# Performance work log

Hardware: AMD Instinct MI355X
Metric: run time of the kernel (lower is better)

The kernel has to match this reference:

```python
import jax, jax.numpy as jnp
import numpy as np

N = 10000       # nodes
E = 320000      # edges (before self-loops)
IN = 16         # in_channels


def _p(key, shape, scale=0.1):
    return jax.random.normal(key, shape, jnp.float32) * scale


def setup_inputs() -> dict:
    key = jax.random.key(0)
    ks = jax.random.split(key, 26)
    d = {}
    d["x"] = jax.random.normal(ks[0], (N, IN), jnp.float32)
    d["edge_index"] = jax.random.randint(ks[1], (2, E), 0, N, jnp.int32)
    d["JetRawPt"] = jax.random.normal(ks[2], (N, 1), jnp.float32)
    # conv1: GATConv(16 -> 32, heads=8)
    d["W1"] = _p(ks[3], (IN, 8 * 32)); d["a1s"] = _p(ks[4], (8, 32)); d["a1d"] = _p(ks[5], (8, 32)); d["b1"] = jnp.zeros((256,), jnp.float32)
    # conv2: GATConv(256 -> 32, heads=8)
    d["W2"] = _p(ks[6], (256, 8 * 32)); d["a2s"] = _p(ks[7], (8, 32)); d["a2d"] = _p(ks[8], (8, 32)); d["b2"] = jnp.zeros((256,), jnp.float32)
    # conv3: GATConv(256 -> 64, heads=12)
    d["W3"] = _p(ks[9], (256, 12 * 64)); d["a3s"] = _p(ks[10], (12, 64)); d["a3d"] = _p(ks[11], (12, 64)); d["b3"] = jnp.zeros((768,), jnp.float32)
    # linear_final: 256+256+768=1280 -> 1
    d["Wf"] = _p(ks[12], (1280, 1)); d["bf"] = jnp.zeros((1,), jnp.float32)
    # MLP: (16+1)->128->64->1
    d["M1w"] = _p(ks[13], (IN + 1, 128)); d["M1b"] = jnp.zeros((128,), jnp.float32)
    d["M2w"] = _p(ks[14], (128, 64)); d["M2b"] = jnp.zeros((64,), jnp.float32)
    d["M3w"] = _p(ks[15], (64, 1)); d["M3b"] = jnp.zeros((1,), jnp.float32)
    return d


def gat_layer(x, src, dst, W, a_s, a_d, b, H, C):
    # PyG GATConv (eval mode, self-loops already appended to src/dst)
    h = (x @ W).reshape(-1, H, C)                      # [N, H, C]
    al = jnp.sum(h * a_s, axis=-1)                     # [N, H] src-side score
    ar = jnp.sum(h * a_d, axis=-1)                     # [N, H] dst-side score
    e = jax.nn.leaky_relu(al[src] + ar[dst], 0.2)      # [Etot, H]
    m = jax.ops.segment_max(e, dst, num_segments=N)    # segment softmax over incoming edges
    ex = jnp.exp(e - m[dst])
    s = jax.ops.segment_sum(ex, dst, num_segments=N)
    alpha = ex / s[dst]                                # [Etot, H]
    out = jax.ops.segment_sum(h[src] * alpha[:, :, None], dst, num_segments=N)  # [N, H, C]
    return out.reshape(-1, H * C) + b


def reference(x, edge_index, JetRawPt, W1, a1s, a1d, b1, W2, a2s, a2d, b2,
              W3, a3s, a3d, b3, Wf, bf, M1w, M1b, M2w, M2b, M3w, M3b):
    loops = jnp.arange(N, dtype=edge_index.dtype)
    src = jnp.concatenate([edge_index[0], loops])
    dst = jnp.concatenate([edge_index[1], loops])
    x1 = jax.nn.relu(gat_layer(x, src, dst, W1, a1s, a1d, b1, 8, 32))
    x2 = jax.nn.relu(gat_layer(x1, src, dst, W2, a2s, a2d, b2, 8, 32))
    x3 = jax.nn.relu(gat_layer(x2, src, dst, W3, a3s, a3d, b3, 12, 64))
    xc = jnp.concatenate([x1, x2, x3], axis=1)         # [N, 1280]
    out1 = jax.nn.sigmoid(xc @ Wf + bf)                # [N, 1]
    xm = jnp.concatenate([x, out1], axis=1)            # [N, 17]
    h = jax.nn.relu(xm @ M1w + M1b)
    h = jax.nn.relu(h @ M2w + M2b)
    out2 = jax.nn.sigmoid(h @ M3w + M3b)               # [N, 1]
    return (out1, out2)
```

## Files before the change

### kernel.cpp

```cpp
#include <hip/hip_runtime.h>
#include <math.h>


typedef unsigned short bf16_t;
typedef __attribute__((ext_vector_type(8))) short bf16x8;
typedef __attribute__((ext_vector_type(4))) float f32x4;
typedef __attribute__((ext_vector_type(2))) float f32x2;

__device__ inline float bf2f(bf16_t u) {
    union { unsigned int i; float f; } v; v.i = ((unsigned int)u) << 16; return v.f;
}
__device__ inline float u2f(unsigned int x) {
    union { unsigned int i; float f; } v; v.i = x; return v.f;
}
__device__ inline bf16_t f2bf(float f) {
    union { float f; unsigned int i; } v; v.f = f;
    unsigned int r = v.i + 0x7FFF + ((v.i >> 16) & 1);
    return (bf16_t)(r >> 16);
}


__global__ void count_edges(const int* __restrict__ ei, int E, int Nn,
                            int* __restrict__ counts) {
    int e = blockIdx.x * blockDim.x + threadIdx.x;
    if (e >= E + Nn) return;
    int dst = (e < E) ? ei[E + e] : (e - E);
    atomicAdd(&counts[dst], 1);
}

__global__ __launch_bounds__(1024) void scan_rowptr(const int* __restrict__ counts,
                                                    int* __restrict__ rowptr, int n) {
    const int IPT = (n + 1023) / 1024;
    int t = threadIdx.x;
    int base = t * IPT;
    int loc[16];
    int run = 0;
#pragma unroll
    for (int i = 0; i < 16; i++) {
        if (i >= IPT) break;
        int idx = base + i;
        int v = (idx < n) ? counts[idx] : 0;
        loc[i] = run;
        run += v;
    }
    int lane = t & 63, wid = t >> 6;
    int v = run;
    for (int off = 1; off < 64; off <<= 1) {
        int u = __shfl_up(v, off, 64);
        if (lane >= off) v += u;
    }
    __shared__ int wsum[16];
    __shared__ int woff[16];
    if (lane == 63) wsum[wid] = v;
    __syncthreads();
    if (t == 0) { int s = 0; for (int i = 0; i < 16; i++) { woff[i] = s; s += wsum[i]; } }
    __syncthreads();
    int excl = v - run + woff[wid];
#pragma unroll
    for (int i = 0; i < 16; i++) {
        if (i >= IPT) break;
        int idx = base + i;
        if (idx < n) rowptr[idx] = excl + loc[i];
    }
    if (t == 1023) rowptr[n] = excl + run;
}

__global__ void fill_edges(const int* __restrict__ ei, int E, int Nn,
                           const int* __restrict__ rowptr, int* __restrict__ cursor,
                           int* __restrict__ edge_src) {
    int e = blockIdx.x * blockDim.x + threadIdx.x;
    if (e >= E + Nn) return;
    int src, dst;
    if (e < E) { src = ei[e]; dst = ei[E + e]; }
    else       { src = e - E; dst = src; }
    int pos = atomicAdd(&cursor[dst], 1);
    edge_src[rowptr[dst] + pos] = src;
}

__global__ __launch_bounds__(256) void transpose_cast2(const float* __restrict__ W2,
                                                       bf16_t* __restrict__ Wt2,
                                                       const float* __restrict__ W3,
                                                       bf16_t* __restrict__ Wt3) {
    __shared__ float tile[16][17];
    const float* W; bf16_t* Wt; int Nc, n0;
    if (blockIdx.y < 16) { W = W2; Wt = Wt2; Nc = 256; n0 = blockIdx.y * 16; }
    else                 { W = W3; Wt = Wt3; Nc = 768; n0 = (blockIdx.y - 16) * 16; }
    int k0 = blockIdx.x * 16;
    int tx = threadIdx.x & 15, ty = threadIdx.x >> 4;
    tile[ty][tx] = W[(size_t)(k0 + ty) * Nc + n0 + tx];
    __syncthreads();
    Wt[(size_t)(n0 + ty) * 256 + k0 + tx] = f2bf(tile[tx][ty]);
}

__global__ __launch_bounds__(256) void gemm_f32_sc(const float* __restrict__ A,
                                                   const float* __restrict__ B,
                                                   bf16_t* __restrict__ Cm,
                                                   const float* __restrict__ a_s,
                                                   const float* __restrict__ a_d,
                                                   float* __restrict__ al,
                                                   float* __restrict__ ar,
                                                   int M, int K, int Nc, int H) {
    __shared__ float As[16][64];
    __shared__ float Bs[16][64];
    int t  = threadIdx.x;
    int tx = t & 15, ty = t >> 4;
    int row0 = blockIdx.y * 64, col0 = blockIdx.x * 64;
    int a_r = t >> 2, a_c = (t & 3) * 4;
    int b_r = t >> 4, b_c = (t & 15) * 4;

    float acc[4][4];
#pragma unroll
    for (int i = 0; i < 4; i++)
#pragma unroll
        for (int j = 0; j < 4; j++) acc[i][j] = 0.f;

    for (int kt = 0; kt < K; kt += 16) {
        float4 av = make_float4(0.f, 0.f, 0.f, 0.f);
        int gr = row0 + a_r;
        if (gr < M) av = *(const float4*)(A + (size_t)gr * K + kt + a_c);
        As[a_c + 0][a_r] = av.x;
        As[a_c + 1][a_r] = av.y;
        As[a_c + 2][a_r] = av.z;
        As[a_c + 3][a_r] = av.w;
        float4 bv = *(const float4*)(B + (size_t)(kt + b_r) * Nc + col0 + b_c);
        *(float4*)&Bs[b_r][b_c] = bv;
        __syncthreads();
#pragma unroll
        for (int k = 0; k < 16; k++) {
            float4 a4 = *(const float4*)&As[k][ty * 4];
            float4 b4 = *(const float4*)&Bs[k][tx * 4];
            float aa[4] = {a4.x, a4.y, a4.z, a4.w};
            float bb[4] = {b4.x, b4.y, b4.z, b4.w};
#pragma unroll
            for (int i = 0; i < 4; i++)
#pragma unroll
                for (int j = 0; j < 4; j++) acc[i][j] += aa[i] * bb[j];
        }
        __syncthreads();
    }
    float4 asv = *(const float4*)(a_s + col0 + tx * 4);
    float4 adv = *(const float4*)(a_d + col0 + tx * 4);
#pragma unroll
    for (int i = 0; i < 4; i++) {
        int gr = row0 + ty * 4 + i;
        float sa = acc[i][0] * asv.x + acc[i][1] * asv.y + acc[i][2] * asv.z + acc[i][3] * asv.w;
        float sd = acc[i][0] * adv.x + acc[i][1] * adv.y + acc[i][2] * adv.z + acc[i][3] * adv.w;
#pragma unroll
        for (int off = 4; off > 0; off >>= 1) {
            sa += __shfl_xor(sa, off, 64);
            sd += __shfl_xor(sd, off, 64);
        }
        if ((tx == 0 || tx == 8) && gr < M) {
            int h = (col0 >> 5) + (tx >> 3);
            al[gr * H + h] = sa;
            ar[gr * H + h] = sd;
        }
        if (gr < M) {
            ushort4 v;
            v.x = f2bf(acc[i][0]); v.y = f2bf(acc[i][1]);
            v.z = f2bf(acc[i][2]); v.w = f2bf(acc[i][3]);
            *(ushort4*)(Cm + (size_t)gr * Nc + col0 + tx * 4) = v;
        }
    }
}

template <int C_>
__global__ __launch_bounds__(256) void gemm_mfma_sc(const bf16_t* __restrict__ A,
                                                    const bf16_t* __restrict__ Bt,
                                                    bf16_t* __restrict__ Cm,
                                                    const float* __restrict__ a_s,
                                                    const float* __restrict__ a_d,
                                                    float* __restrict__ al,
                                                    float* __restrict__ ar,
                                                    int M, int K, int Nc, int H) {
    int wave = threadIdx.x >> 6, lane = threadIdx.x & 63;
    int quad = lane >> 4, l16 = lane & 15;
    int m0 = blockIdx.y * 128 + wave * 32;
    int n0 = blockIdx.x * 64;

    f32x4 acc[2][4];
    f32x4 z = {0.f, 0.f, 0.f, 0.f};
#pragma unroll
    for (int i = 0; i < 2; i++)
#pragma unroll
        for (int j = 0; j < 4; j++) acc[i][j] = z;

    int r0 = m0 + l16;       if (r0 >= M) r0 = M - 1;
    int r1 = m0 + 16 + l16;  if (r1 >= M) r1 = M - 1;
    const bf16_t* Ap0 = A + (size_t)r0 * K + quad * 8;
    const bf16_t* Ap1 = A + (size_t)r1 * K + quad * 8;
    const bf16_t* Bp0 = Bt + (size_t)(n0 + 0  + l16) * K + quad * 8;
    const bf16_t* Bp1 = Bt + (size_t)(n0 + 16 + l16) * K + quad * 8;
    const bf16_t* Bp2 = Bt + (size_t)(n0 + 32 + l16) * K + quad * 8;
    const bf16_t* Bp3 = Bt + (size_t)(n0 + 48 + l16) * K + quad * 8;

    for (int kt = 0; kt < K; kt += 32) {
        bf16x8 a0 = *(const bf16x8*)(Ap0 + kt);
        bf16x8 a1 = *(const bf16x8*)(Ap1 + kt);
        bf16x8 b0 = *(const bf16x8*)(Bp0 + kt);
        bf16x8 b1 = *(const bf16x8*)(Bp1 + kt);
        bf16x8 b2 = *(const bf16x8*)(Bp2 + kt);
        bf16x8 b3 = *(const bf16x8*)(Bp3 + kt);
        acc[0][0] = __builtin_amdgcn_mfma_f32_16x16x32_bf16(a0, b0, acc[0][0], 0, 0, 0);
        acc[1][0] = __builtin_amdgcn_mfma_f32_16x16x32_bf16(a1, b0, acc[1][0], 0, 0, 0);
        acc[0][1] = __builtin_amdgcn_mfma_f32_16x16x32_bf16(a0, b1, acc[0][1], 0, 0, 0);
        acc[1][1] = __builtin_amdgcn_mfma_f32_16x16x32_bf16(a1, b1, acc[1][1], 0, 0, 0);
        acc[0][2] = __builtin_amdgcn_mfma_f32_16x16x32_bf16(a0, b2, acc[0][2], 0, 0, 0);
        acc[1][2] = __builtin_amdgcn_mfma_f32_16x16x32_bf16(a1, b2, acc[1][2], 0, 0, 0);
        acc[0][3] = __builtin_amdgcn_mfma_f32_16x16x32_bf16(a0, b3, acc[0][3], 0, 0, 0);
        acc[1][3] = __builtin_amdgcn_mfma_f32_16x16x32_bf16(a1, b3, acc[1][3], 0, 0, 0);
    }

    float asv[4], adv[4];
#pragma unroll
    for (int j = 0; j < 4; j++) {
        asv[j] = a_s[n0 + j * 16 + l16];
        adv[j] = a_d[n0 + j * 16 + l16];
    }
#pragma unroll
    for (int i = 0; i < 2; i++)
#pragma unroll
        for (int r = 0; r < 4; r++) {
            int gr = m0 + i * 16 + quad * 4 + r;
            if (C_ == 64) {
                float sa = acc[i][0][r] * asv[0] + acc[i][1][r] * asv[1]
                         + acc[i][2][r] * asv[2] + acc[i][3][r] * asv[3];
                float sd = acc[i][0][r] * adv[0] + acc[i][1][r] * adv[1]
                         + acc[i][2][r] * adv[2] + acc[i][3][r] * adv[3];
#pragma unroll
                for (int off = 8; off > 0; off >>= 1) {
                    sa += __shfl_xor(sa, off, 64);
                    sd += __shfl_xor(sd, off, 64);
                }
                if (l16 == 0 && gr < M) {
                    int h = n0 >> 6;
                    al[gr * H + h] = sa;
                    ar[gr * H + h] = sd;
                }
            } else {
                float saA = acc[i][0][r] * asv[0] + acc[i][1][r] * asv[1];
                float saB = acc[i][2][r] * asv[2] + acc[i][3][r] * asv[3];
                float sdA = acc[i][0][r] * adv[0] + acc[i][1][r] * adv[1];
                float sdB = acc[i][2][r] * adv[2] + acc[i][3][r] * adv[3];
#pragma unroll
                for (int off = 8; off > 0; off >>= 1) {
                    saA += __shfl_xor(saA, off, 64);
                    saB += __shfl_xor(saB, off, 64);
                    sdA += __shfl_xor(sdA, off, 64);
                    sdB += __shfl_xor(sdB, off, 64);
                }
                if (l16 == 0 && gr < M) {
                    int h = n0 >> 5;
                    al[gr * H + h]     = saA;
                    ar[gr * H + h]     = sdA;
                    al[gr * H + h + 1] = saB;
                    ar[gr * H + h + 1] = sdB;
                }
            }
        }
#pragma unroll
    for (int i = 0; i < 2; i++)
#pragma unroll
        for (int j = 0; j < 4; j++)
#pragma unroll
            for (int r = 0; r < 4; r++) {
                int gr = m0 + i * 16 + quad * 4 + r;
                if (gr < M) Cm[(size_t)gr * Nc + n0 + j * 16 + l16] = f2bf(acc[i][j][r]);
            }
}

template <int HC_, int C, int H>
__global__ __launch_bounds__(256) void gat_agg_fused(
    const bf16_t* __restrict__ hbuf, const float* __restrict__ al,
    const float* __restrict__ ar, const int* __restrict__ rowptr,
    const int* __restrict__ esrc, const float* __restrict__ bias,
    bf16_t* __restrict__ outb, int n, int nodeblocks) {
    constexpr int HPG = 128 / C;
    __shared__ float plds[4][128 * HPG];
    int group = blockIdx.x / nodeblocks;
    int nb    = blockIdx.x - group * nodeblocks;
    int wv    = threadIdx.x >> 6;
    int node  = nb * 4 + wv;
    if (node >= n) return;
    int lane  = threadIdx.x & 63;
    int ghead = group * HPG;

    int beg = rowptr[node], end = rowptr[node + 1];
    int deg = end - beg;

    int e0 = 0, e1 = 0;
    {
        int i0 = beg + lane;
        if (i0 < end) e0 = esrc[i0];
        int i1 = beg + 64 + lane;
        if (i1 < end) e1 = esrc[i1];
    }
    int npre  = deg < 128 ? deg : 128;
    int nfull = (npre + 7) >> 3;

    float arv[HPG];
#pragma unroll
    for (int t = 0; t < HPG; t++) arv[t] = ar[(size_t)node * H + ghead + t];
    float s[HPG];
#pragma unroll
    for (int t = 0; t < HPG; t++) s[t] = 0.f;
    float* pw = plds[wv];
    {
        int jz = deg + lane;
        if (jz < (nfull << 3)) {
#pragma unroll
            for (int t = 0; t < HPG; t++) pw[jz * HPG + t] = 0.f;
        }
    }
    for (int k = 0; k < deg; k += 64) {
        int j = k + lane;
        if (j < deg) {
            int src = (k == 0) ? e0 : ((k == 64) ? e1 : esrc[beg + j]);
            const float* alr = al + (size_t)src * H + ghead;
            float p[HPG];
#pragma unroll
            for (int t = 0; t < HPG; t++) {
                float e = alr[t] + arv[t];
                e = fmaxf(e, 0.2f * e);
                p[t] = __expf(fminf(e, 60.f));
                s[t] += p[t];
            }
            if (j < 128) {
#pragma unroll
                for (int t = 0; t < HPG; t++) pw[j * HPG + t] = p[t];
            }
        }
    }
#pragma unroll
    for (int t = 0; t < HPG; t++) {
        float v = s[t];
#pragma unroll
        for (int off = 32; off > 0; off >>= 1) v += __shfl_xor(v, off, 64);
        s[t] = 1.f / v;
    }

    int sub = lane >> 4, cl = lane & 15;
    int gc  = group * 128 + cl * 8;
    int t_local = (cl * 8) / C;
    float inv_local, arv_local;
    if (HPG == 2) {
        inv_local = t_local ? s[1] : s[0];
        arv_local = t_local ? arv[1] : arv[0];
    } else {
        float iv0 = t_local & 1 ? s[1] : s[0];
        float iv1 = t_local & 1 ? s[3] : s[2];
        inv_local = (t_local & 2) ? iv1 : iv0;
        float av0 = t_local & 1 ? arv[1] : arv[0];
        float av1 = t_local & 1 ? arv[3] : arv[2];
        arv_local = (t_local & 2) ? av1 : av0;
    }
    const bf16_t* hb = hbuf + gc;

    f32x2 acc2[4];
    f32x2 z2 = {0.f, 0.f};
#pragma unroll
    for (int i = 0; i < 4; i++) acc2[i] = z2;

    if (nfull > 0) {
        int s0 = __shfl(e0, sub, 64);
        int s1 = __shfl(e0, sub + 4, 64);
        float a0 = pw[sub * HPG + t_local];
        float a1 = pw[(sub + 4) * HPG + t_local];
        bf16x8 u0 = *(const bf16x8*)(hb + (size_t)s0 * HC_);
        bf16x8 u1 = *(const bf16x8*)(hb + (size_t)s1 * HC_);
        for (int it = 1; it < nfull; ++it) {
            int kb = it * 8;
            int esel = (kb < 64) ? e0 : e1;
            int t0 = __shfl(esel, (kb + sub) & 63, 64);
            int t1 = __shfl(esel, (kb + sub + 4) & 63, 64);
            float b0v = pw[(kb + sub) * HPG + t_local];
            float b1v = pw[(kb + sub + 4) * HPG + t_local];
            bf16x8 v0 = *(const bf16x8*)(hb + (size_t)t0 * HC_);
            bf16x8 v1 = *(const bf16x8*)(hb + (size_t)t1 * HC_);
            const unsigned int* d0 = (const unsigned int*)&u0;
            const unsigned int* d1 = (const unsigned int*)&u1;
            f32x2 a0v = {a0, a0}, a1v = {a1, a1};
#pragma unroll
            for (int i = 0; i < 4; i++) {
                f32x2 w0 = {u2f(d0[i] << 16), u2f(d0[i] & 0xffff0000u)};
                f32x2 w1 = {u2f(d1[i] << 16), u2f(d1[i] & 0xffff0000u)};
                acc2[i] += a0v * w0;
                acc2[i] += a1v * w1;
            }
            u0 = v0; u1 = v1; a0 = b0v; a1 = b1v;
        }
        const unsigned int* d0 = (const unsigned int*)&u0;
        const unsigned int* d1 = (const unsigned int*)&u1;
        f32x2 a0v = {a0, a0}, a1v = {a1, a1};
#pragma unroll
        for (int i = 0; i < 4; i++) {
            f32x2 w0 = {u2f(d0[i] << 16), u2f(d0[i] & 0xffff0000u)};
            f32x2 w1 = {u2f(d1[i] << 16), u2f(d1[i] & 0xffff0000u)};
            acc2[i] += a0v * w0;
            acc2[i] += a1v * w1;
        }
    }
    for (int j = beg + (nfull << 3) + sub; j < end; j += 4) {
        int s0 = esrc[j];
        float e = al[(size_t)s0 * H + ghead + t_local] + arv_local;
        e = fmaxf(e, 0.2f * e);
        float a0 = __expf(fminf(e, 60.f));
        bf16x8 u0 = *(const bf16x8*)(hb + (size_t)s0 * HC_);
        const unsigned int* d0 = (const unsigned int*)&u0;
        f32x2 a0v = {a0, a0};
#pragma unroll
        for (int i = 0; i < 4; i++) {
            f32x2 w0 = {u2f(d0[i] << 16), u2f(d0[i] & 0xffff0000u)};
            acc2[i] += a0v * w0;
        }
    }
    float acc[8] = {acc2[0].x, acc2[0].y, acc2[1].x, acc2[1].y,
                    acc2[2].x, acc2[2].y, acc2[3].x, acc2[3].y};
#pragma unroll
    for (int i = 0; i < 8; i++) {
        acc[i] += __shfl_xor(acc[i], 16, 64);
        acc[i] += __shfl_xor(acc[i], 32, 64);
    }
    if (sub == 0) {
        float4 b0 = *(const float4*)(bias + gc);
        float4 b1 = *(const float4*)(bias + gc + 4);
        float bb[8] = {b0.x, b0.y, b0.z, b0.w, b1.x, b1.y, b1.z, b1.w};
        bf16x8 outv;
        unsigned short* ov = (unsigned short*)&outv;
#pragma unroll
        for (int i = 0; i < 8; i++) ov[i] = f2bf(fmaxf(acc[i] * inv_local + bb[i], 0.f));
        *(bf16x8*)(outb + (size_t)node * HC_ + gc) = outv;
    }
}

__global__ __launch_bounds__(256) void head_fused(
    const float* __restrict__ x, const bf16_t* __restrict__ x1b,
    const bf16_t* __restrict__ x2b, const bf16_t* __restrict__ x3b,
    const float* __restrict__ Wf, const float* __restrict__ bfc,
    const float* __restrict__ M1w, const float* __restrict__ M1b,
    const float* __restrict__ M2w, const float* __restrict__ M2b,
    const float* __restrict__ M3w, const float* __restrict__ M3b,
    float* __restrict__ out1, float* __restrict__ out2, int n) {
    __shared__ float h1s[4][128];
    int w    = threadIdx.x >> 6;
    int lane = threadIdx.x & 63;
    int node = blockIdx.x * 4 + w;
    bool valid = node < n;
    int nd = valid ? node : 0;

    float s = 0.f;
    {
        ushort4 u = *(const ushort4*)(x1b + (size_t)nd * 256 + lane * 4);
        const float* wv = Wf + lane * 4;
        s += bf2f(u.x) * wv[0] + bf2f(u.y) * wv[1] + bf2f(u.z) * wv[2] + bf2f(u.w) * wv[3];
    }
    {
        ushort4 u = *(const ushort4*)(x2b + (size_t)nd * 256 + lane * 4);
        const float* wv = Wf + 256 + lane * 4;
        s += bf2f(u.x) * wv[0] + bf2f(u.y) * wv[1] + bf2f(u.z) * wv[2] + bf2f(u.w) * wv[3];
    }
#pragma unroll
    for (int i = 0; i < 3; i++) {
        int k = i * 256 + lane * 4;
        ushort4 u = *(const ushort4*)(x3b + (size_t)nd * 768 + k);
        const float* wv = Wf + 512 + k;
        s += bf2f(u.x) * wv[0] + bf2f(u.y) * wv[1] + bf2f(u.z) * wv[2] + bf2f(u.w) * wv[3];
    }
#pragma unroll
    for (int off = 32; off > 0; off >>= 1) s += __shfl_xor(s, off, 64);
    float so = 1.f / (1.f + __expf(-(s + bfc[0])));
    if (lane == 0 && valid) out1[node] = so;

    float xm[17];
#pragma unroll
    for (int k = 0; k < 16; k++) xm[k] = x[nd * 16 + k];
    xm[16] = so;

    float a0 = M1b[lane], a1 = M1b[lane + 64];
#pragma unroll
    for (int k = 0; k < 17; k++) {
        a0 += xm[k] * M1w[k * 128 + lane];
        a1 += xm[k] * M1w[k * 128 + lane + 64];
    }
    h1s[w][lane]      = fmaxf(a0, 0.f);
    h1s[w][lane + 64] = fmaxf(a1, 0.f);
    __syncthreads();

    float b0 = M2b[lane];
#pragma unroll 16
    for (int k = 0; k < 128; k++) b0 += h1s[w][k] * M2w[k * 64 + lane];
    b0 = fmaxf(b0, 0.f);

    float p = b0 * M3w[lane];
#pragma unroll
    for (int off = 32; off > 0; off >>= 1) p += __shfl_xor(p, off, 64);
    if (lane == 0 && valid) out2[node] = 1.f / (1.f + __expf(-(p + M3b[0])));
}

extern "C" void kernel_launch(void* const* d_in, const int* in_sizes, int n_in,
                              void* d_out, int out_size, void* d_ws, size_t ws_size,
                              hipStream_t stream) {
    const float* x   = (const float*)d_in[0];
    const int*   ei  = (const int*)d_in[1];
    const float* W1  = (const float*)d_in[3];
    const float* a1s = (const float*)d_in[4];
    const float* a1d = (const float*)d_in[5];
    const float* b1  = (const float*)d_in[6];
    const float* W2  = (const float*)d_in[7];
    const float* a2s = (const float*)d_in[8];
    const float* a2d = (const float*)d_in[9];
    const float* b2  = (const float*)d_in[10];
    const float* W3  = (const float*)d_in[11];
    const float* a3s = (const float*)d_in[12];
    const float* a3d = (const float*)d_in[13];
    const float* b3  = (const float*)d_in[14];
    const float* Wf  = (const float*)d_in[15];
    const float* bf  = (const float*)d_in[16];
    const float* M1w = (const float*)d_in[17];
    const float* M1b = (const float*)d_in[18];
    const float* M2w = (const float*)d_in[19];
    const float* M2b = (const float*)d_in[20];
    const float* M3w = (const float*)d_in[21];
    const float* M3b = (const float*)d_in[22];

    const int N = in_sizes[0] / 16;
    const int E = in_sizes[1] / 2;
    const int Etot = E + N;

    char* base = (char*)d_ws;
    size_t off = 0;
    auto carve = [&](size_t bytes) {
        char* p = base + off;
        off = (off + bytes + 255) & ~(size_t)255;
        return p;
    };
    bf16_t* hbuf   = (bf16_t*)carve((size_t)N * 768 * 2);
    bf16_t* x1b    = (bf16_t*)carve((size_t)N * 256 * 2);
    bf16_t* x2b    = (bf16_t*)carve((size_t)N * 256 * 2);
    bf16_t* x3b    = (bf16_t*)carve((size_t)N * 768 * 2);
    bf16_t* Wt2    = (bf16_t*)carve((size_t)256 * 256 * 2);
    bf16_t* Wt3    = (bf16_t*)carve((size_t)256 * 768 * 2);
    float*  al     = (float*)carve((size_t)N * 12 * 4);
    float*  ar     = (float*)carve((size_t)N * 12 * 4);
    int*    rowptr = (int*)carve((size_t)(N + 1) * 4);
    int*    cnt2   = (int*)carve((size_t)(2 * N) * 4);
    int*    counts = cnt2;
    int*    cursor = cnt2 + N;
    int*    esrc   = (int*)carve((size_t)Etot * 4);
    (void)ws_size;

    float* out1 = (float*)d_out;
    float* out2 = (float*)d_out + N;

    const int TB = 256;
    int eb = (Etot + TB - 1) / TB;
    int nodeblocks = (N + 3) / 4;

    hipMemsetAsync(cnt2, 0, (size_t)(2 * N) * 4, stream);
    count_edges<<<eb, TB, 0, stream>>>(ei, E, N, counts);
    scan_rowptr<<<1, 1024, 0, stream>>>(counts, rowptr, N);
    fill_edges<<<eb, TB, 0, stream>>>(ei, E, N, rowptr, cursor, esrc);
    transpose_cast2<<<dim3(16, 64), TB, 0, stream>>>(W2, Wt2, W3, Wt3);

    gemm_f32_sc<<<dim3(4, (N + 63) / 64), TB, 0, stream>>>(x, W1, hbuf, a1s, a1d, al, ar, N, 16, 256, 8);
    gat_agg_fused<256, 32, 8><<<2 * nodeblocks, TB, 0, stream>>>(hbuf, al, ar, rowptr, esrc, b1, x1b, N, nodeblocks);

    gemm_mfma_sc<32><<<dim3(4, (N + 127) / 128), TB, 0, stream>>>(x1b, Wt2, hbuf, a2s, a2d, al, ar, N, 256, 256, 8);
    gat_agg_fused<256, 32, 8><<<2 * nodeblocks, TB, 0, stream>>>(hbuf, al, ar, rowptr, esrc, b2, x2b, N, nodeblocks);

    gemm_mfma_sc<64><<<dim3(12, (N + 127) / 128), TB, 0, stream>>>(x2b, Wt3, hbuf, a3s, a3d, al, ar, N, 256, 768, 12);
    gat_agg_fused<768, 64, 12><<<6 * nodeblocks, TB, 0, stream>>>(hbuf, al, ar, rowptr, esrc, b3, x3b, N, nodeblocks);

    head_fused<<<nodeblocks, TB, 0, stream>>>(x, x1b, x2b, x3b, Wf, bf,
                                              M1w, M1b, M2w, M2b, M3w, M3b, out1, out2, N);
}
```

Baseline: 309.4 us.

## Prefetch neighbor rows early and deepen gather pipeline in GAT aggregation

The first two bf16 feature-row gathers and the src-side score loads are issued at kernel start, before the softmax-weight computation, so their latency overlaps the exp work. The aggregation loop becomes a two-deep software pipeline that prefetches the iteration two ahead. The softmax-sum reduction and reciprocal move after aggregation, so the reduction no longer sits between the score and gather phases. This costs more live registers (four bf16x8 buffers plus score arrays), which may lower occupancy, and issues loads for invalid lanes that read src index 0.

```diff
diff --git a/kernel.cpp b/kernel.cpp
--- a/kernel.cpp
+++ b/kernel.cpp
@@ -298,6 +298,30 @@
     int npre  = deg < 128 ? deg : 128;
     int nfull = (npre + 7) >> 3;
 
+    const float* alr0 = al + (size_t)e0 * H + ghead;
+    const float* alr1 = al + (size_t)e1 * H + ghead;
+    float alv0[HPG], alv1[HPG];
+#pragma unroll
+    for (int t = 0; t < HPG; t++) alv0[t] = alr0[t];
+#pragma unroll
+    for (int t = 0; t < HPG; t++) alv1[t] = alr1[t];
+
+    int sub = lane >> 4, cl = lane & 15;
+    int gc  = group * 128 + cl * 8;
+    int t_local = (cl * 8) / C;
+    const bf16_t* hb = hbuf + gc;
+    bf16x8 u0, u1, v0, v1;
+    {
+        int s0 = __shfl(e0, sub, 64);
+        int s1 = __shfl(e0, sub + 4, 64);
+        u0 = *(const bf16x8*)(hb + (size_t)s0 * HC_);
+        u1 = *(const bf16x8*)(hb + (size_t)s1 * HC_);
+        int t0 = __shfl(e0, 8 + sub, 64);
+        int t1 = __shfl(e0, 12 + sub, 64);
+        v0 = *(const bf16x8*)(hb + (size_t)t0 * HC_);
+        v1 = *(const bf16x8*)(hb + (size_t)t1 * HC_);
+    }
+
     float arv[HPG];
 #pragma unroll
     for (int t = 0; t < HPG; t++) arv[t] = ar[(size_t)node * H + ghead + t];
@@ -312,83 +336,44 @@
             for (int t = 0; t < HPG; t++) pw[jz * HPG + t] = 0.f;
         }
     }
-    for (int k = 0; k < deg; k += 64) {
+    bool ok0 = lane < deg;
+    bool ok1 = 64 + lane < deg;
+#pragma unroll
+    for (int t = 0; t < HPG; t++) {
+        float e = alv0[t] + arv[t];
+        e = fmaxf(e, 0.2f * e);
+        float p = __expf(fminf(e, 60.f));
+        if (ok0) { pw[lane * HPG + t] = p; s[t] += p; }
+    }
+#pragma unroll
+    for (int t = 0; t < HPG; t++) {
+        float e = alv1[t] + arv[t];
+        e = fmaxf(e, 0.2f * e);
+        float p = __expf(fminf(e, 60.f));
+        if (ok1) { pw[(64 + lane) * HPG + t] = p; s[t] += p; }
+    }
+    for (int k = 128; k < deg; k += 64) {
         int j = k + lane;
         if (j < deg) {
-            int src = (k == 0) ? e0 : ((k == 64) ? e1 : esrc[beg + j]);
-            const float* alr = al + (size_t)src * H + ghead;
-            float p[HPG];
+            const float* alr = al + (size_t)esrc[beg + j] * H + ghead;
 #pragma unroll
             for (int t = 0; t < HPG; t++) {
                 float e = alr[t] + arv[t];
                 e = fmaxf(e, 0.2f * e);
-                p[t] = __expf(fminf(e, 60.f));
-                s[t] += p[t];
+                s[t] += __expf(fminf(e, 60.f));
             }
-            if (j < 128) {
-#pragma unroll
-                for (int t = 0; t < HPG; t++) pw[j * HPG + t] = p[t];
-            }
-        }
-    }
-#pragma unroll
-    for (int t = 0; t < HPG; t++) {
-        float v = s[t];
-#pragma unroll
-        for (int off = 32; off > 0; off >>= 1) v += __shfl_xor(v, off, 64);
-        s[t] = 1.f / v;
-    }
-
-    int sub = lane >> 4, cl = lane & 15;
-    int gc  = group * 128 + cl * 8;
-    int t_local = (cl * 8) / C;
-    float inv_local, arv_local;
-    if (HPG == 2) {
-        inv_local = t_local ? s[1] : s[0];
-        arv_local = t_local ? arv[1] : arv[0];
-    } else {
-        float iv0 = t_local & 1 ? s[1] : s[0];
-        float iv1 = t_local & 1 ? s[3] : s[2];
-        inv_local = (t_local & 2) ? iv1 : iv0;
-        float av0 = t_local & 1 ? arv[1] : arv[0];
-        float av1 = t_local & 1 ? arv[3] : arv[2];
-        arv_local = (t_local & 2) ? av1 : av0;
-    }
-    const bf16_t* hb = hbuf + gc;
+        }
+    }
 
     f32x2 acc2[4];
     f32x2 z2 = {0.f, 0.f};
 #pragma unroll
     for (int i = 0; i < 4; i++) acc2[i] = z2;
 
-    if (nfull > 0) {
-        int s0 = __shfl(e0, sub, 64);
-        int s1 = __shfl(e0, sub + 4, 64);
-        float a0 = pw[sub * HPG + t_local];
-        float a1 = pw[(sub + 4) * HPG + t_local];
-        bf16x8 u0 = *(const bf16x8*)(hb + (size_t)s0 * HC_);
-        bf16x8 u1 = *(const bf16x8*)(hb + (size_t)s1 * HC_);
-        for (int it = 1; it < nfull; ++it) {
-            int kb = it * 8;
-            int esel = (kb < 64) ? e0 : e1;
-            int t0 = __shfl(esel, (kb + sub) & 63, 64);
-            int t1 = __shfl(esel, (kb + sub + 4) & 63, 64);
-            float b0v = pw[(kb + sub) * HPG + t_local];
-            float b1v = pw[(kb + sub + 4) * HPG + t_local];
-            bf16x8 v0 = *(const bf16x8*)(hb + (size_t)t0 * HC_);
-            bf16x8 v1 = *(const bf16x8*)(hb + (size_t)t1 * HC_);
-            const unsigned int* d0 = (const unsigned int*)&u0;
-            const unsigned int* d1 = (const unsigned int*)&u1;
-            f32x2 a0v = {a0, a0}, a1v = {a1, a1};
-#pragma unroll
-            for (int i = 0; i < 4; i++) {
-                f32x2 w0 = {u2f(d0[i] << 16), u2f(d0[i] & 0xffff0000u)};
-                f32x2 w1 = {u2f(d1[i] << 16), u2f(d1[i] & 0xffff0000u)};
-                acc2[i] += a0v * w0;
-                acc2[i] += a1v * w1;
-            }
-            u0 = v0; u1 = v1; a0 = b0v; a1 = b1v;
-        }
+    for (int it = 0; it < nfull; ++it) {
+        int kb = it * 8;
+        float a0 = pw[(kb + sub) * HPG + t_local];
+        float a1 = pw[(kb + sub + 4) * HPG + t_local];
         const unsigned int* d0 = (const unsigned int*)&u0;
         const unsigned int* d1 = (const unsigned int*)&u1;
         f32x2 a0v = {a0, a0}, a1v = {a1, a1};
@@ -399,20 +384,54 @@
             acc2[i] += a0v * w0;
             acc2[i] += a1v * w1;
         }
+        u0 = v0; u1 = v1;
+        int nx = it + 2;
+        if (nx < nfull) {
+            int kb2 = nx * 8;
+            int esel = (kb2 & 64) ? e1 : e0;
+            int t0 = __shfl(esel, (kb2 + sub) & 63, 64);
+            int t1 = __shfl(esel, (kb2 + sub + 4) & 63, 64);
+            v0 = *(const bf16x8*)(hb + (size_t)t0 * HC_);
+            v1 = *(const bf16x8*)(hb + (size_t)t1 * HC_);
+        }
+    }
+    float arv_local;
+    if (HPG == 2) {
+        arv_local = t_local ? arv[1] : arv[0];
+    } else {
+        float av0 = (t_local & 1) ? arv[1] : arv[0];
+        float av1 = (t_local & 1) ? arv[3] : arv[2];
+        arv_local = (t_local & 2) ? av1 : av0;
     }
     for (int j = beg + (nfull << 3) + sub; j < end; j += 4) {
         int s0 = esrc[j];
         float e = al[(size_t)s0 * H + ghead + t_local] + arv_local;
         e = fmaxf(e, 0.2f * e);
         float a0 = __expf(fminf(e, 60.f));
-        bf16x8 u0 = *(const bf16x8*)(hb + (size_t)s0 * HC_);
-        const unsigned int* d0 = (const unsigned int*)&u0;
+        bf16x8 u0t = *(const bf16x8*)(hb + (size_t)s0 * HC_);
+        const unsigned int* d0 = (const unsigned int*)&u0t;
         f32x2 a0v = {a0, a0};
 #pragma unroll
         for (int i = 0; i < 4; i++) {
             f32x2 w0 = {u2f(d0[i] << 16), u2f(d0[i] & 0xffff0000u)};
             acc2[i] += a0v * w0;
         }
+    }
+
+#pragma unroll
+    for (int t = 0; t < HPG; t++) {
+        float v = s[t];
+#pragma unroll
+        for (int off = 32; off > 0; off >>= 1) v += __shfl_xor(v, off, 64);
+        s[t] = 1.f / v;
+    }
+    float inv_local;
+    if (HPG == 2) {
+        inv_local = t_local ? s[1] : s[0];
+    } else {
+        float iv0 = (t_local & 1) ? s[1] : s[0];
+        float iv1 = (t_local & 1) ? s[3] : s[2];
+        inv_local = (t_local & 2) ? iv1 : iv0;
     }
     float acc[8] = {acc2[0].x, acc2[0].y, acc2[1].x, acc2[1].y,
                     acc2[2].x, acc2[2].y, acc2[3].x, acc2[3].y};
```

Result: no change. 309.4 us (+0.0%).
